# Kernel optimization log

Hardware: AMD Instinct MI355X
Metric: run time of the kernel (lower is better)

Reference implementation:

```python
import jax, jax.numpy as jnp
import numpy as np

LOSS_WEIGHT = 0.1  # config.mvot.discrepancy_loss_weight


def setup_inputs() -> dict:
    key = jax.random.key(0)
    k1, k2, k3, k4, k5 = jax.random.split(key, 5)
    B, S, H, K = 2, 2048, 1024, 16384
    return {
        "hidden_states": jax.random.normal(k1, (B, S, H), dtype=jnp.float32),
        "token_type_ids": jax.random.randint(k2, (B, S), 0, 2, dtype=jnp.int64),
        "target_embeddings": jax.random.normal(k3, (B, S, H), dtype=jnp.float32),
        "W_proj": jax.random.normal(k4, (K, H), dtype=jnp.float32) * (1.0 / np.sqrt(H)),
        "b_proj": jnp.zeros((K,), dtype=jnp.float32),
        "codebook": jax.random.normal(k5, (K, H), dtype=jnp.float32),
    }


def reference(hidden_states, token_type_ids, target_embeddings, W_proj, b_proj, codebook):
    B, S, H = hidden_states.shape
    K, D = codebook.shape
    mask = (token_type_ids == 1).reshape(-1).astype(hidden_states.dtype)  # [N]
    x = hidden_states.reshape(-1, H)          # [N, H]
    t = target_embeddings.reshape(-1, D)      # [N, D]

    # token_projection + softmax
    logits = x @ W_proj.T + b_proj            # [N, K]
    probs = jax.nn.softmax(logits, axis=-1)

    # mean squared distance to every codebook entry:
    # mean_d (t - c)^2 = (||t||^2 - 2 t.c + ||c||^2) / D
    t_sq = jnp.sum(t * t, axis=-1, keepdims=True)          # [N, 1]
    c_sq = jnp.sum(codebook * codebook, axis=-1)           # [K]
    cross = t @ codebook.T                                 # [N, K]
    mse_distances = (t_sq - 2.0 * cross + c_sq) / D        # [N, K]

    # mask-weighted sum == torch boolean-mask-then-sum
    per_token = jnp.sum(mse_distances * probs, axis=-1)    # [N]
    loss = jnp.sum(per_token * mask) * LOSS_WEIGHT
    return loss
```

## Files before the change

### kernel.cpp

```cpp
#include <hip/hip_runtime.h>
#include <hip/hip_bf16.h>
#include <math.h>

#define LOSS_WEIGHT 0.1f

typedef unsigned short u16;
typedef __bf16 bf16x8 __attribute__((ext_vector_type(8)));
typedef float f32x4 __attribute__((ext_vector_type(4)));

__device__ __forceinline__ void gload_lds16(const void* gsrc, void* ldst) {
    const __attribute__((address_space(1))) unsigned int* g =
        reinterpret_cast<const __attribute__((address_space(1))) unsigned int*>(
            reinterpret_cast<uintptr_t>(gsrc));
    __attribute__((address_space(3))) unsigned int* l =
        reinterpret_cast<__attribute__((address_space(3))) unsigned int*>(
            reinterpret_cast<uintptr_t>(ldst));
    __builtin_amdgcn_global_load_lds(g, l, 16, 0, 0);
}

__device__ __forceinline__ u16 f2b(float f) {
    __bf16 b = (__bf16)f;
    return __builtin_bit_cast(u16, b);
}

__global__ __launch_bounds__(256) void gather_kernel(
    const int* __restrict__ tti, int* __restrict__ idx_list,
    int* __restrict__ count, int N)
{
    int n = blockIdx.x * blockDim.x + threadIdx.x;
    if (n < N && tti[n] == 1) {
        int pos = atomicAdd(count, 1);
        idx_list[pos] = n;
    }
}

__global__ __launch_bounds__(256) void prep_kernel(
    const float* __restrict__ x, const float* __restrict__ t,
    const float* __restrict__ W, const float* __restrict__ C,
    const int* __restrict__ idx_list, const int* __restrict__ count,
    u16* __restrict__ xb, u16* __restrict__ tb,
    u16* __restrict__ wb, u16* __restrict__ cb,
    float* __restrict__ t_sq, float* __restrict__ c_sq,
    int N, int K, int H)
{
    const int rid = blockIdx.x;

    if (rid < N) {
        const int cnt  = *count;
        const int cntp = (cnt + 63) & ~63;
        if (rid >= cntp) return;
        u16* ox = xb + (size_t)rid * H;
        u16* ot = tb + (size_t)rid * H;
        if (rid >= cnt) {
            for (int h = threadIdx.x * 4; h < H; h += blockDim.x * 4) {
                *(uint2*)(ox + h) = (uint2){0u, 0u};
                *(uint2*)(ot + h) = (uint2){0u, 0u};
            }
            if (threadIdx.x == 0) t_sq[rid] = 0.f;
            return;
        }
        const int src_row = idx_list[rid];
        const float* rx = x + (size_t)src_row * H;
        const float* rt = t + (size_t)src_row * H;
        float acc = 0.f;
        for (int h = threadIdx.x * 4; h < H; h += blockDim.x * 4) {
            float4 vx = *(const float4*)(rx + h);
            float4 vt = *(const float4*)(rt + h);
            acc += vt.x*vt.x + vt.y*vt.y + vt.z*vt.z + vt.w*vt.w;
            uint2 px, pt;
            px.x = (unsigned)f2b(vx.x) | ((unsigned)f2b(vx.y) << 16);
            px.y = (unsigned)f2b(vx.z) | ((unsigned)f2b(vx.w) << 16);
            pt.x = (unsigned)f2b(vt.x) | ((unsigned)f2b(vt.y) << 16);
            pt.y = (unsigned)f2b(vt.z) | ((unsigned)f2b(vt.w) << 16);
            *(uint2*)(ox + h) = px;
            *(uint2*)(ot + h) = pt;
        }
        #pragma unroll
        for (int s = 1; s < 64; s <<= 1) acc += __shfl_xor(acc, s);
        __shared__ float wpart[4];
        if ((threadIdx.x & 63) == 0) wpart[threadIdx.x >> 6] = acc;
        __syncthreads();
        if (threadIdx.x == 0) t_sq[rid] = wpart[0] + wpart[1] + wpart[2] + wpart[3];
        return;
    }

    const int wrid = rid - N;
    const float* src; u16* dst; float* sq = nullptr; int row;
    if (wrid < K) { src = W; dst = wb; row = wrid; }
    else          { src = C; dst = cb; row = wrid - K; sq = c_sq; }

    const float* r = src + (size_t)row * H;
    u16* o = dst + (size_t)row * H;
    float acc = 0.f;
    for (int h = threadIdx.x * 4; h < H; h += blockDim.x * 4) {
        float4 v = *(const float4*)(r + h);
        acc += v.x*v.x + v.y*v.y + v.z*v.z + v.w*v.w;
        uint2 pk;
        pk.x = (unsigned)f2b(v.x) | ((unsigned)f2b(v.y) << 16);
        pk.y = (unsigned)f2b(v.z) | ((unsigned)f2b(v.w) << 16);
        *(uint2*)(o + h) = pk;
    }
    if (sq) {
        #pragma unroll
        for (int s = 1; s < 64; s <<= 1) acc += __shfl_xor(acc, s);
        __shared__ float wpart2[4];
        if ((threadIdx.x & 63) == 0) wpart2[threadIdx.x >> 6] = acc;
        __syncthreads();
        if (threadIdx.x == 0) sq[row] = wpart2[0] + wpart2[1] + wpart2[2] + wpart2[3];
    }
}

__global__ __launch_bounds__(256) void fused_gemm_kernel(
    const u16* __restrict__ xb, const u16* __restrict__ tb,
    const u16* __restrict__ wb, const u16* __restrict__ cb,
    const float* __restrict__ b_proj, const float* __restrict__ t_sq,
    const float* __restrict__ c_sq, const int* __restrict__ count,
    float* __restrict__ pm, float* __restrict__ ps, float* __restrict__ pw,
    int H, float invD)
{
    const int mb = blockIdx.y;
    const int m0 = mb * 64;
    {
        const int cnt = *count;
        if (m0 >= ((cnt + 63) & ~63)) return;
    }

    __shared__ u16 xs[64 * 64];
    __shared__ u16 ts[64 * 64];
    __shared__ u16 ws[128 * 64];
    __shared__ u16 cs[128 * 64];

    const int tid  = threadIdx.x;
    const int lane = tid & 63;
    const int wv   = tid >> 6;
    const int kb   = blockIdx.x;
    const int KB   = gridDim.x;
    const int k0   = kb * 128;

    f32x4 accL[8], accC[8];
    #pragma unroll
    for (int i = 0; i < 8; ++i) {
        accL[i] = (f32x4){0.f, 0.f, 0.f, 0.f};
        accC[i] = (f32x4){0.f, 0.f, 0.f, 0.f};
    }

    const int kx    = (lane & 7) << 4;
    const int koff0 = (((lane >> 4) << 4)) ^ kx;
    const int koff1 = (64 + ((lane >> 4) << 4)) ^ kx;
    const char* xs_b = (const char*)xs + (wv * 16 + (lane & 15)) * 128;
    const char* ts_b = (const char*)ts + (wv * 16 + (lane & 15)) * 128;
    const char* ws_b = (const char*)ws + (lane & 15) * 128;
    const char* cs_b = (const char*)cs + (lane & 15) * 128;

    const int e0 = tid * 8;

    for (int h0 = 0; h0 < H; h0 += 64) {
        #pragma unroll
        for (int j = 0; j < 2; ++j) {
            int el  = j * 2048 + e0;
            int es  = el ^ (((el >> 6) & 7) << 3);
            int row = es >> 6, col = es & 63;
            gload_lds16(xb + (size_t)(m0 + row) * H + h0 + col, (u16*)xs + el);
            gload_lds16(tb + (size_t)(m0 + row) * H + h0 + col, (u16*)ts + el);
        }
        #pragma unroll
        for (int j = 0; j < 4; ++j) {
            int el  = j * 2048 + e0;
            int es  = el ^ (((el >> 6) & 7) << 3);
            int row = es >> 6, col = es & 63;
            gload_lds16(wb + (size_t)(k0 + row) * H + h0 + col, (u16*)ws + el);
            gload_lds16(cb + (size_t)(k0 + row) * H + h0 + col, (u16*)cs + el);
        }
        __syncthreads();

        #pragma unroll
        for (int kk = 0; kk < 2; ++kk) {
            const int ko = kk ? koff1 : koff0;
            bf16x8 ax = *(const bf16x8*)(xs_b + ko);
            bf16x8 at = *(const bf16x8*)(ts_b + ko);
            #pragma unroll
            for (int nf = 0; nf < 8; ++nf) {
                bf16x8 bw = *(const bf16x8*)(ws_b + nf * 2048 + ko);
                bf16x8 bc = *(const bf16x8*)(cs_b + nf * 2048 + ko);
                accL[nf] = __builtin_amdgcn_mfma_f32_16x16x32_bf16(ax, bw, accL[nf], 0, 0, 0);
                accC[nf] = __builtin_amdgcn_mfma_f32_16x16x32_bf16(at, bc, accC[nf], 0, 0, 0);
            }
        }
        __syncthreads();
    }

    float bias[8], csq[8];
    #pragma unroll
    for (int nf = 0; nf < 8; ++nf) {
        int c = k0 + nf * 16 + (lane & 15);
        bias[nf] = b_proj[c];
        csq[nf]  = c_sq[c];
    }
    const int rbase = m0 + wv * 16 + ((lane >> 4) << 2);
    #pragma unroll
    for (int j = 0; j < 4; ++j) {
        const int row = rbase + j;
        const float tsq = t_sq[row];
        float lg[8], ms[8];
        float mx = -1e30f;
        #pragma unroll
        for (int nf = 0; nf < 8; ++nf) {
            lg[nf] = accL[nf][j] + bias[nf];
            ms[nf] = (tsq - 2.f * accC[nf][j] + csq[nf]) * invD;
            mx = fmaxf(mx, lg[nf]);
        }
        #pragma unroll
        for (int s = 1; s < 16; s <<= 1) mx = fmaxf(mx, __shfl_xor(mx, s));
        float esum = 0.f, wsum = 0.f;
        #pragma unroll
        for (int nf = 0; nf < 8; ++nf) {
            float e = __expf(lg[nf] - mx);
            esum += e;
            wsum += e * ms[nf];
        }
        #pragma unroll
        for (int s = 1; s < 16; s <<= 1) {
            esum += __shfl_xor(esum, s);
            wsum += __shfl_xor(wsum, s);
        }
        if ((lane & 15) == 0) {
            size_t idx = (size_t)row * KB + kb;
            pm[idx] = mx; ps[idx] = esum; pw[idx] = wsum;
        }
    }
}

__global__ __launch_bounds__(256) void finalize_kernel(
    const float* __restrict__ pm, const float* __restrict__ ps,
    const float* __restrict__ pw, const int* __restrict__ count,
    float* __restrict__ out, int KB)
{
    const int lane = threadIdx.x & 63;
    const int wv   = threadIdx.x >> 6;
    const int tok  = blockIdx.x * 4 + wv;
    const int cnt  = *count;
    float contrib = 0.f;
    if (tok < cnt) {
        const size_t base = (size_t)tok * KB;
        float m = -1e30f;
        for (int i = lane; i < KB; i += 64) m = fmaxf(m, pm[base + i]);
        #pragma unroll
        for (int s = 1; s < 64; s <<= 1) m = fmaxf(m, __shfl_xor(m, s));
        float esum = 0.f, wsum = 0.f;
        for (int i = lane; i < KB; i += 64) {
            float sc = __expf(pm[base + i] - m);
            esum += ps[base + i] * sc;
            wsum += pw[base + i] * sc;
        }
        #pragma unroll
        for (int s = 1; s < 64; s <<= 1) {
            esum += __shfl_xor(esum, s);
            wsum += __shfl_xor(wsum, s);
        }
        contrib = wsum / esum;
    }
    __shared__ float bsum[4];
    if (lane == 0) bsum[wv] = contrib;
    __syncthreads();
    if (threadIdx.x == 0) {
        float v = (bsum[0] + bsum[1] + bsum[2] + bsum[3]) * LOSS_WEIGHT;
        atomicAdd(out, v);
    }
}

extern "C" void kernel_launch(void* const* d_in, const int* in_sizes, int n_in,
                              void* d_out, int out_size, void* d_ws, size_t ws_size,
                              hipStream_t stream)
{
    const float* x   = (const float*)d_in[0];
    const int*   tti = (const int*)d_in[1];
    const float* t   = (const float*)d_in[2];
    const float* W   = (const float*)d_in[3];
    const float* b   = (const float*)d_in[4];
    const float* C   = (const float*)d_in[5];

    const int N  = in_sizes[1];
    const int K  = in_sizes[4];
    const int H  = in_sizes[0] / N;
    const int KB = K / 128;

    char* p = (char*)d_ws;
    auto alloc = [&](size_t bytes) {
        char* r = p;
        p += (bytes + 255) & ~(size_t)255;
        return r;
    };
    u16*   xb   = (u16*)alloc((size_t)N * H * 2);
    u16*   tb   = (u16*)alloc((size_t)N * H * 2);
    u16*   wb   = (u16*)alloc((size_t)K * H * 2);
    u16*   cb   = (u16*)alloc((size_t)K * H * 2);
    float* t_sq = (float*)alloc((size_t)N * 4);
    float* c_sq = (float*)alloc((size_t)K * 4);
    float* pm   = (float*)alloc((size_t)N * KB * 4);
    float* ps   = (float*)alloc((size_t)N * KB * 4);
    float* pw   = (float*)alloc((size_t)N * KB * 4);
    int*   ilist= (int*)alloc((size_t)N * 4);
    int*   cnt  = (int*)alloc(4);

    hipMemsetAsync(d_out, 0, sizeof(float), stream);
    hipMemsetAsync(cnt, 0, sizeof(int), stream);

    gather_kernel<<<(N + 255) / 256, 256, 0, stream>>>(tti, ilist, cnt, N);

    prep_kernel<<<N + 2 * K, 256, 0, stream>>>(
        x, t, W, C, ilist, cnt, xb, tb, wb, cb, t_sq, c_sq, N, K, H);

    dim3 grid(K / 128, N / 64);
    fused_gemm_kernel<<<grid, 256, 0, stream>>>(
        xb, tb, wb, cb, b, t_sq, c_sq, cnt, pm, ps, pw, H, 1.f / (float)H);

    finalize_kernel<<<(N + 3) / 4, 256, 0, stream>>>(
        pm, ps, pw, cnt, (float*)d_out, KB);
}
```

Baseline: 388.0 us.

## Enlarge GEMM tile to 128x128 with 2x2 wave layout; one row per wave in prep

The fused dual-GEMM now uses a 128x128 output tile per block, with the four waves in a 2x2 arrangement each computing a 64x64 sub-tile (16 MFMA accumulators per GEMM). This raises arithmetic intensity and cuts redundant global/LDS traffic for the weight and codebook tiles. Partial softmax statistics are now written per 64-column half, so the finalize kernel reads twice as many partials. The prep kernel also changes to one row per wave with 16-byte stores, which removes block-level syncs. The cost is higher register pressure from 32 accumulator vectors and fewer blocks in the grid.

```diff
diff --git a/kernel.cpp b/kernel.cpp
--- a/kernel.cpp
+++ b/kernel.cpp
@@ -22,6 +22,9 @@
     __bf16 b = (__bf16)f;
     return __builtin_bit_cast(u16, b);
 }
+__device__ __forceinline__ unsigned pack2(float a, float b) {
+    return (unsigned)f2b(a) | ((unsigned)f2b(b) << 16);
+}
 
 __global__ __launch_bounds__(256) void gather_kernel(
     const int* __restrict__ tti, int* __restrict__ idx_list,
@@ -43,74 +46,75 @@
     float* __restrict__ t_sq, float* __restrict__ c_sq,
     int N, int K, int H)
 {
-    const int rid = blockIdx.x;
-
-    if (rid < N) {
+    const int lane = threadIdx.x & 63;
+    const int wv   = threadIdx.x >> 6;
+    const int NT   = N >> 2, KQ = K >> 2;
+    const int bid  = blockIdx.x;
+
+    if (bid < NT) {
+        const int rid  = bid * 4 + wv;
         const int cnt  = *count;
-        const int cntp = (cnt + 63) & ~63;
+        const int cntp = (cnt + 127) & ~127;
         if (rid >= cntp) return;
         u16* ox = xb + (size_t)rid * H;
         u16* ot = tb + (size_t)rid * H;
         if (rid >= cnt) {
-            for (int h = threadIdx.x * 4; h < H; h += blockDim.x * 4) {
-                *(uint2*)(ox + h) = (uint2){0u, 0u};
-                *(uint2*)(ot + h) = (uint2){0u, 0u};
-            }
-            if (threadIdx.x == 0) t_sq[rid] = 0.f;
+            for (int p = lane * 8; p < H; p += 512) {
+                *(uint4*)(ox + p) = (uint4){0u, 0u, 0u, 0u};
+                *(uint4*)(ot + p) = (uint4){0u, 0u, 0u, 0u};
+            }
+            if (lane == 0) t_sq[rid] = 0.f;
             return;
         }
         const int src_row = idx_list[rid];
         const float* rx = x + (size_t)src_row * H;
         const float* rt = t + (size_t)src_row * H;
         float acc = 0.f;
-        for (int h = threadIdx.x * 4; h < H; h += blockDim.x * 4) {
-            float4 vx = *(const float4*)(rx + h);
-            float4 vt = *(const float4*)(rt + h);
-            acc += vt.x*vt.x + vt.y*vt.y + vt.z*vt.z + vt.w*vt.w;
-            uint2 px, pt;
-            px.x = (unsigned)f2b(vx.x) | ((unsigned)f2b(vx.y) << 16);
-            px.y = (unsigned)f2b(vx.z) | ((unsigned)f2b(vx.w) << 16);
-            pt.x = (unsigned)f2b(vt.x) | ((unsigned)f2b(vt.y) << 16);
-            pt.y = (unsigned)f2b(vt.z) | ((unsigned)f2b(vt.w) << 16);
-            *(uint2*)(ox + h) = px;
-            *(uint2*)(ot + h) = pt;
+        for (int p = lane * 8; p < H; p += 512) {
+            float4 xa = *(const float4*)(rx + p);
+            float4 xbv = *(const float4*)(rx + p + 4);
+            float4 ta = *(const float4*)(rt + p);
+            float4 tbv = *(const float4*)(rt + p + 4);
+            acc += ta.x*ta.x + ta.y*ta.y + ta.z*ta.z + ta.w*ta.w
+                 + tbv.x*tbv.x + tbv.y*tbv.y + tbv.z*tbv.z + tbv.w*tbv.w;
+            uint4 px = {pack2(xa.x, xa.y), pack2(xa.z, xa.w),
+                        pack2(xbv.x, xbv.y), pack2(xbv.z, xbv.w)};
+            uint4 pt = {pack2(ta.x, ta.y), pack2(ta.z, ta.w),
+                        pack2(tbv.x, tbv.y), pack2(tbv.z, tbv.w)};
+            *(uint4*)(ox + p) = px;
+            *(uint4*)(ot + p) = pt;
         }
         #pragma unroll
         for (int s = 1; s < 64; s <<= 1) acc += __shfl_xor(acc, s);
-        __shared__ float wpart[4];
-        if ((threadIdx.x & 63) == 0) wpart[threadIdx.x >> 6] = acc;
-        __syncthreads();
-        if (threadIdx.x == 0) t_sq[rid] = wpart[0] + wpart[1] + wpart[2] + wpart[3];
+        if (lane == 0) t_sq[rid] = acc;
         return;
     }
 
-    const int wrid = rid - N;
+    const int wbid = bid - NT;
     const float* src; u16* dst; float* sq = nullptr; int row;
-    if (wrid < K) { src = W; dst = wb; row = wrid; }
-    else          { src = C; dst = cb; row = wrid - K; sq = c_sq; }
+    if (wbid < KQ) { src = W; dst = wb; row = wbid * 4 + wv; }
+    else           { src = C; dst = cb; row = (wbid - KQ) * 4 + wv; sq = c_sq; }
 
     const float* r = src + (size_t)row * H;
     u16* o = dst + (size_t)row * H;
     float acc = 0.f;
-    for (int h = threadIdx.x * 4; h < H; h += blockDim.x * 4) {
-        float4 v = *(const float4*)(r + h);
-        acc += v.x*v.x + v.y*v.y + v.z*v.z + v.w*v.w;
-        uint2 pk;
-        pk.x = (unsigned)f2b(v.x) | ((unsigned)f2b(v.y) << 16);
-        pk.y = (unsigned)f2b(v.z) | ((unsigned)f2b(v.w) << 16);
-        *(uint2*)(o + h) = pk;
+    for (int p = lane * 8; p < H; p += 512) {
+        float4 a = *(const float4*)(r + p);
+        float4 b = *(const float4*)(r + p + 4);
+        acc += a.x*a.x + a.y*a.y + a.z*a.z + a.w*a.w
+             + b.x*b.x + b.y*b.y + b.z*b.z + b.w*b.w;
+        uint4 pk = {pack2(a.x, a.y), pack2(a.z, a.w),
+                    pack2(b.x, b.y), pack2(b.z, b.w)};
+        *(uint4*)(o + p) = pk;
     }
     if (sq) {
         #pragma unroll
         for (int s = 1; s < 64; s <<= 1) acc += __shfl_xor(acc, s);
-        __shared__ float wpart2[4];
-        if ((threadIdx.x & 63) == 0) wpart2[threadIdx.x >> 6] = acc;
-        __syncthreads();
-        if (threadIdx.x == 0) sq[row] = wpart2[0] + wpart2[1] + wpart2[2] + wpart2[3];
-    }
-}
-
-__global__ __launch_bounds__(256) void fused_gemm_kernel(
+        if (lane == 0) sq[row] = acc;
+    }
+}
+
+__global__ __launch_bounds__(256, 2) void fused_gemm_kernel(
     const u16* __restrict__ xb, const u16* __restrict__ tb,
     const u16* __restrict__ wb, const u16* __restrict__ cb,
     const float* __restrict__ b_proj, const float* __restrict__ t_sq,
@@ -119,27 +123,29 @@
     int H, float invD)
 {
     const int mb = blockIdx.y;
-    const int m0 = mb * 64;
+    const int m0 = mb * 128;
     {
         const int cnt = *count;
-        if (m0 >= ((cnt + 63) & ~63)) return;
-    }
-
-    __shared__ u16 xs[64 * 64];
-    __shared__ u16 ts[64 * 64];
+        if (m0 >= ((cnt + 127) & ~127)) return;
+    }
+
+    __shared__ u16 xs[128 * 64];
+    __shared__ u16 ts[128 * 64];
     __shared__ u16 ws[128 * 64];
     __shared__ u16 cs[128 * 64];
 
     const int tid  = threadIdx.x;
     const int lane = tid & 63;
     const int wv   = tid >> 6;
+    const int wr   = wv >> 1;
+    const int wc   = wv & 1;
     const int kb   = blockIdx.x;
-    const int KB   = gridDim.x;
+    const int KB2  = gridDim.x * 2;
     const int k0   = kb * 128;
 
-    f32x4 accL[8], accC[8];
+    f32x4 accL[16], accC[16];
     #pragma unroll
-    for (int i = 0; i < 8; ++i) {
+    for (int i = 0; i < 16; ++i) {
         accL[i] = (f32x4){0.f, 0.f, 0.f, 0.f};
         accC[i] = (f32x4){0.f, 0.f, 0.f, 0.f};
     }
@@ -147,27 +153,21 @@
     const int kx    = (lane & 7) << 4;
     const int koff0 = (((lane >> 4) << 4)) ^ kx;
     const int koff1 = (64 + ((lane >> 4) << 4)) ^ kx;
-    const char* xs_b = (const char*)xs + (wv * 16 + (lane & 15)) * 128;
-    const char* ts_b = (const char*)ts + (wv * 16 + (lane & 15)) * 128;
-    const char* ws_b = (const char*)ws + (lane & 15) * 128;
-    const char* cs_b = (const char*)cs + (lane & 15) * 128;
+    const char* xs_b = (const char*)xs + (wr * 64 + (lane & 15)) * 128;
+    const char* ts_b = (const char*)ts + (wr * 64 + (lane & 15)) * 128;
+    const char* ws_b = (const char*)ws + (wc * 64 + (lane & 15)) * 128;
+    const char* cs_b = (const char*)cs + (wc * 64 + (lane & 15)) * 128;
 
     const int e0 = tid * 8;
 
     for (int h0 = 0; h0 < H; h0 += 64) {
         #pragma unroll
-        for (int j = 0; j < 2; ++j) {
+        for (int j = 0; j < 4; ++j) {
             int el  = j * 2048 + e0;
             int es  = el ^ (((el >> 6) & 7) << 3);
             int row = es >> 6, col = es & 63;
             gload_lds16(xb + (size_t)(m0 + row) * H + h0 + col, (u16*)xs + el);
             gload_lds16(tb + (size_t)(m0 + row) * H + h0 + col, (u16*)ts + el);
-        }
-        #pragma unroll
-        for (int j = 0; j < 4; ++j) {
-            int el  = j * 2048 + e0;
-            int es  = el ^ (((el >> 6) & 7) << 3);
-            int row = es >> 6, col = es & 63;
             gload_lds16(wb + (size_t)(k0 + row) * H + h0 + col, (u16*)ws + el);
             gload_lds16(cb + (size_t)(k0 + row) * H + h0 + col, (u16*)cs + el);
         }
@@ -176,56 +176,68 @@
         #pragma unroll
         for (int kk = 0; kk < 2; ++kk) {
             const int ko = kk ? koff1 : koff0;
-            bf16x8 ax = *(const bf16x8*)(xs_b + ko);
-            bf16x8 at = *(const bf16x8*)(ts_b + ko);
-            #pragma unroll
-            for (int nf = 0; nf < 8; ++nf) {
-                bf16x8 bw = *(const bf16x8*)(ws_b + nf * 2048 + ko);
-                bf16x8 bc = *(const bf16x8*)(cs_b + nf * 2048 + ko);
-                accL[nf] = __builtin_amdgcn_mfma_f32_16x16x32_bf16(ax, bw, accL[nf], 0, 0, 0);
-                accC[nf] = __builtin_amdgcn_mfma_f32_16x16x32_bf16(at, bc, accC[nf], 0, 0, 0);
+            bf16x8 ax[4], at[4], bw[4], bc[4];
+            #pragma unroll
+            for (int i = 0; i < 4; ++i) {
+                ax[i] = *(const bf16x8*)(xs_b + i * 2048 + ko);
+                at[i] = *(const bf16x8*)(ts_b + i * 2048 + ko);
+                bw[i] = *(const bf16x8*)(ws_b + i * 2048 + ko);
+                bc[i] = *(const bf16x8*)(cs_b + i * 2048 + ko);
+            }
+            #pragma unroll
+            for (int mi = 0; mi < 4; ++mi) {
+                #pragma unroll
+                for (int ni = 0; ni < 4; ++ni) {
+                    accL[mi * 4 + ni] = __builtin_amdgcn_mfma_f32_16x16x32_bf16(
+                        ax[mi], bw[ni], accL[mi * 4 + ni], 0, 0, 0);
+                    accC[mi * 4 + ni] = __builtin_amdgcn_mfma_f32_16x16x32_bf16(
+                        at[mi], bc[ni], accC[mi * 4 + ni], 0, 0, 0);
+                }
             }
         }
         __syncthreads();
     }
 
-    float bias[8], csq[8];
+    float bias[4], csq[4];
     #pragma unroll
-    for (int nf = 0; nf < 8; ++nf) {
-        int c = k0 + nf * 16 + (lane & 15);
-        bias[nf] = b_proj[c];
-        csq[nf]  = c_sq[c];
-    }
-    const int rbase = m0 + wv * 16 + ((lane >> 4) << 2);
+    for (int ni = 0; ni < 4; ++ni) {
+        int c = k0 + wc * 64 + ni * 16 + (lane & 15);
+        bias[ni] = b_proj[c];
+        csq[ni]  = c_sq[c];
+    }
+    const int rbase = m0 + wr * 64 + ((lane >> 4) << 2);
     #pragma unroll
-    for (int j = 0; j < 4; ++j) {
-        const int row = rbase + j;
-        const float tsq = t_sq[row];
-        float lg[8], ms[8];
-        float mx = -1e30f;
-        #pragma unroll
-        for (int nf = 0; nf < 8; ++nf) {
-            lg[nf] = accL[nf][j] + bias[nf];
-            ms[nf] = (tsq - 2.f * accC[nf][j] + csq[nf]) * invD;
-            mx = fmaxf(mx, lg[nf]);
-        }
-        #pragma unroll
-        for (int s = 1; s < 16; s <<= 1) mx = fmaxf(mx, __shfl_xor(mx, s));
-        float esum = 0.f, wsum = 0.f;
-        #pragma unroll
-        for (int nf = 0; nf < 8; ++nf) {
-            float e = __expf(lg[nf] - mx);
-            esum += e;
-            wsum += e * ms[nf];
-        }
-        #pragma unroll
-        for (int s = 1; s < 16; s <<= 1) {
-            esum += __shfl_xor(esum, s);
-            wsum += __shfl_xor(wsum, s);
-        }
-        if ((lane & 15) == 0) {
-            size_t idx = (size_t)row * KB + kb;
-            pm[idx] = mx; ps[idx] = esum; pw[idx] = wsum;
+    for (int mi = 0; mi < 4; ++mi) {
+        #pragma unroll
+        for (int j = 0; j < 4; ++j) {
+            const int row = rbase + mi * 16 + j;
+            const float tsq = t_sq[row];
+            float lg[4], ms[4];
+            float mx = -1e30f;
+            #pragma unroll
+            for (int ni = 0; ni < 4; ++ni) {
+                lg[ni] = accL[mi * 4 + ni][j] + bias[ni];
+                ms[ni] = (tsq - 2.f * accC[mi * 4 + ni][j] + csq[ni]) * invD;
+                mx = fmaxf(mx, lg[ni]);
+            }
+            #pragma unroll
+            for (int s = 1; s < 16; s <<= 1) mx = fmaxf(mx, __shfl_xor(mx, s));
+            float esum = 0.f, wsum = 0.f;
+            #pragma unroll
+            for (int ni = 0; ni < 4; ++ni) {
+                float e = __expf(lg[ni] - mx);
+                esum += e;
+                wsum += e * ms[ni];
+            }
+            #pragma unroll
+            for (int s = 1; s < 16; s <<= 1) {
+                esum += __shfl_xor(esum, s);
+                wsum += __shfl_xor(wsum, s);
+            }
+            if ((lane & 15) == 0) {
+                size_t idx = (size_t)row * KB2 + kb * 2 + wc;
+                pm[idx] = mx; ps[idx] = esum; pw[idx] = wsum;
+            }
         }
     }
 }
@@ -233,7 +245,7 @@
 __global__ __launch_bounds__(256) void finalize_kernel(
     const float* __restrict__ pm, const float* __restrict__ ps,
     const float* __restrict__ pw, const int* __restrict__ count,
-    float* __restrict__ out, int KB)
+    float* __restrict__ out, int KB2)
 {
     const int lane = threadIdx.x & 63;
     const int wv   = threadIdx.x >> 6;
@@ -241,13 +253,13 @@
     const int cnt  = *count;
     float contrib = 0.f;
     if (tok < cnt) {
-        const size_t base = (size_t)tok * KB;
+        const size_t base = (size_t)tok * KB2;
         float m = -1e30f;
-        for (int i = lane; i < KB; i += 64) m = fmaxf(m, pm[base + i]);
+        for (int i = lane; i < KB2; i += 64) m = fmaxf(m, pm[base + i]);
         #pragma unroll
         for (int s = 1; s < 64; s <<= 1) m = fmaxf(m, __shfl_xor(m, s));
         float esum = 0.f, wsum = 0.f;
-        for (int i = lane; i < KB; i += 64) {
+        for (int i = lane; i < KB2; i += 64) {
             float sc = __expf(pm[base + i] - m);
             esum += ps[base + i] * sc;
             wsum += pw[base + i] * sc;
@@ -279,10 +291,10 @@
     const float* b   = (const float*)d_in[4];
     const float* C   = (const float*)d_in[5];
 
-    const int N  = in_sizes[1];
-    const int K  = in_sizes[4];
-    const int H  = in_sizes[0] / N;
-    const int KB = K / 128;
+    const int N   = in_sizes[1];
+    const int K   = in_sizes[4];
+    const int H   = in_sizes[0] / N;
+    const int KB2 = K / 64;
 
     char* p = (char*)d_ws;
     auto alloc = [&](size_t bytes) {
@@ -296,9 +308,9 @@
     u16*   cb   = (u16*)alloc((size_t)K * H * 2);
     float* t_sq = (float*)alloc((size_t)N * 4);
     float* c_sq = (float*)alloc((size_t)K * 4);
-    float* pm   = (float*)alloc((size_t)N * KB * 4);
-    float* ps   = (float*)alloc((size_t)N * KB * 4);
-    float* pw   = (float*)alloc((size_t)N * KB * 4);
+    float* pm   = (float*)alloc((size_t)N * KB2 * 4);
+    float* ps   = (float*)alloc((size_t)N * KB2 * 4);
+    float* pw   = (float*)alloc((size_t)N * KB2 * 4);
     int*   ilist= (int*)alloc((size_t)N * 4);
     int*   cnt  = (int*)alloc(4);
 
@@ -307,13 +319,13 @@
 
     gather_kernel<<<(N + 255) / 256, 256, 0, stream>>>(tti, ilist, cnt, N);
 
-    prep_kernel<<<N + 2 * K, 256, 0, stream>>>(
+    prep_kernel<<<N / 4 + K / 2, 256, 0, stream>>>(
         x, t, W, C, ilist, cnt, xb, tb, wb, cb, t_sq, c_sq, N, K, H);
 
-    dim3 grid(K / 128, N / 64);
+    dim3 grid(K / 128, N / 128);
     fused_gemm_kernel<<<grid, 256, 0, stream>>>(
         xb, tb, wb, cb, b, t_sq, c_sq, cnt, pm, ps, pw, H, 1.f / (float)H);
 
     finalize_kernel<<<(N + 3) / 4, 256, 0, stream>>>(
-        pm, ps, pw, cnt, (float*)d_out, KB);
-}
+        pm, ps, pw, cnt, (float*)d_out, KB2);
+}
```

New measurement: 385.9 us. About the same (-0.5%).
